# Optimization experiments

Measured on AMD Instinct MI355X. Metric: run time of the kernel, lower is better.

Reference implementation:

```python
import jax, jax.numpy as jnp
import numpy as np

B_, L_, O_, N_, S_, U_, DEL, HID, K = 16, 128, 128, 256, 64, 32, 64, 512, 4
D_OUT = DEL + N_ * U_ + N_ * S_  # 24640


def setup_inputs() -> dict:
    key = jax.random.key(0)
    ks = jax.random.split(key, 12)
    return {
        "x": jax.random.normal(ks[0], (B_, O_ + L_, S_), jnp.float32),
        "u": jax.random.normal(ks[1], (B_, 2 * L_, U_), jnp.float32),
        "A": jax.random.normal(ks[2], (N_, 1), jnp.float32) / 20.0,
        "W0": jax.random.normal(ks[3], (HID, S_), jnp.float32) * 0.05,
        "b0": jnp.zeros((HID,), jnp.float32),
        "W1": jax.random.normal(ks[4], (N_, HID), jnp.float32) * 0.05,
        "b1": jnp.zeros((N_,), jnp.float32),
        "conv_w": jax.random.normal(ks[5], (N_ + U_, 1, K), jnp.float32) * 0.3,
        "conv_b": jnp.zeros((N_ + U_,), jnp.float32),
        "Wg": jax.random.normal(ks[6], (D_OUT, N_ + U_), jnp.float32) * 0.05,
        "bg": jnp.zeros((D_OUT,), jnp.float32),
        "Wdt": jax.random.normal(ks[7], (N_, DEL), jnp.float32) * 0.05,
        "bdt": jnp.zeros((N_,), jnp.float32),
    }


def reference(x, u, A, W0, b0, W1, b1, conv_w, conv_b, Wg, bg, Wdt, bdt):
    def proj_x(v):  # Linear -> relu -> Linear (project_x)
        return jax.nn.relu(v @ W0.T + b0) @ W1.T + b1

    u = u[:, :, :U_]
    z0 = proj_x(x[:, O_ - 1, :])                       # (B, N)

    # ---- generate_matrices ----
    x_all = proj_x(x[:, :O_ - 1, :])                   # (B, O-1, N)
    u_all = u[:, :O_ - 1, :]                           # (B, O-1, U)
    old = jax.nn.silu(jnp.concatenate([x_all, u_all], axis=2))  # (B, O-1, N+U)
    old = jnp.transpose(old, (0, 2, 1))                # (B, N+U, O-1)
    old = jax.lax.conv_general_dilated(
        old, conv_w, window_strides=(1,), padding=[(K - 1, K - 1)],
        dimension_numbers=("NCH", "OIH", "NCH"), feature_group_count=N_ + U_,
    ) + conv_b[None, :, None]
    old = old[:, :, -L_:]                              # last L timesteps
    old = jax.nn.silu(jnp.transpose(old, (0, 2, 1)))   # (B, L, N+U)
    gen = old @ Wg.T + bg                              # (B, L, delta + N*U + N*S)
    delta, Bm, Cm = jnp.split(gen, [DEL, DEL + N_ * U_], axis=-1)
    delta = jax.nn.softplus(delta @ Wdt.T + bdt)       # (B, L, N)
    Bm = Bm.reshape(B_, L_, N_, U_)
    Cm = Cm.reshape(B_, L_, N_, S_)

    # ---- discretion_matrices ----
    a = A[:, 0]
    a = -jnp.where(a > 0, a, jnp.expm1(a))             # -celu(A), alpha=1
    dA = jnp.exp(delta * a)                            # (B, L, N)
    dB = ((dA - 1.0) * (1.0 / a))[..., None] * Bm      # (B, L, N, U)

    # ---- selective_scan ----
    u0 = u[:, O_ - 1:O_ - 1 + L_, :]                   # (B, L, U)
    xt = x[:, O_:O_ + L_, :]                           # (B, L, S) targets

    def step(z, inp):
        dAi, dBi, ui, Ci, xti = inp
        z = z * dAi + jnp.einsum("bnu,bu->bn", dBi, ui)
        y = jnp.einsum("bns,bn->bs", Ci, z)
        return z, (y, jnp.mean((y - xti) ** 2))

    xs = (
        jnp.swapaxes(dA, 0, 1), jnp.swapaxes(dB, 0, 1),
        jnp.swapaxes(u0, 0, 1), jnp.swapaxes(Cm, 0, 1), jnp.swapaxes(xt, 0, 1),
    )
    _, (ys, ls) = jax.lax.scan(step, z0, xs)
    loss = jnp.sum(ls) / L_
    return loss, jax.lax.stop_gradient(ys)             # ys: (L, B, S), detached as in torch
```

## Files before the change

### kernel.cpp

```cpp
#include <hip/hip_runtime.h>
#include <math.h>

#define B_   16
#define L_   128
#define O_   128
#define N_   256
#define S_   64
#define U_   32
#define DEL_ 64
#define HID_ 512
#define CH_  288
#define M_   2048
#define KD_  288
#define CM_BASE (DEL_ + N_*U_)
#define NSLICE 32

typedef __bf16 bf16_t;
typedef bf16_t bf16x8 __attribute__((ext_vector_type(8)));
typedef float  f32x4  __attribute__((ext_vector_type(4)));

#define AS1(p) ((const __attribute__((address_space(1))) void*)(unsigned long long)(const void*)(p))
#define AS3(p) ((__attribute__((address_space(3))) void*)(unsigned int)(unsigned long long)(const void*)(p))

__device__ __forceinline__ float silu_f(float x){ return x / (1.f + expf(-x)); }
__device__ __forceinline__ float softplus_f(float x){
  return fmaxf(x, 0.f) + log1pf(expf(-fabsf(x)));
}

__device__ __forceinline__ void cvt8(const float* src, bf16_t* dst){
  float4 a = ((const float4*)src)[0];
  float4 b = ((const float4*)src)[1];
  bf16x8 o;
  o[0]=(bf16_t)a.x; o[1]=(bf16_t)a.y; o[2]=(bf16_t)a.z; o[3]=(bf16_t)a.w;
  o[4]=(bf16_t)b.x; o[5]=(bf16_t)b.y; o[6]=(bf16_t)b.z; o[7]=(bf16_t)b.w;
  *(bf16x8*)dst = o;
}

#define CVT_BLOCKS 3465
#define W0_BLOCKS  16
#define W1_BLOCKS  64
#define XB_BLOCKS  64
__global__ void k_prep(const float* __restrict__ Wg, bf16_t* __restrict__ Wgbf,
                       const float* __restrict__ W0, bf16_t* __restrict__ W0bf,
                       const float* __restrict__ W1, bf16_t* __restrict__ W1bf,
                       const float* __restrict__ x,  bf16_t* __restrict__ xbf,
                       float* __restrict__ lossa){
  if (blockIdx.x == 0 && threadIdx.x < 2) lossa[threadIdx.x] = 0.f;
  if (blockIdx.x < CVT_BLOCKS) {
    int i = blockIdx.x*256 + threadIdx.x;
    if (i >= 887040) return;
    cvt8(Wg + (size_t)i*8, Wgbf + (size_t)i*8);
  } else if (blockIdx.x < CVT_BLOCKS + W0_BLOCKS) {
    int i = (blockIdx.x - CVT_BLOCKS)*256 + threadIdx.x;
    if (i >= 4096) return;
    cvt8(W0 + (size_t)i*8, W0bf + (size_t)i*8);
  } else if (blockIdx.x < CVT_BLOCKS + W0_BLOCKS + W1_BLOCKS) {
    int i = (blockIdx.x - CVT_BLOCKS - W0_BLOCKS)*256 + threadIdx.x;
    if (i >= 16384) return;
    cvt8(W1 + (size_t)i*8, W1bf + (size_t)i*8);
  } else {
    int i = (blockIdx.x - CVT_BLOCKS - W0_BLOCKS - W1_BLOCKS)*256 + threadIdx.x;
    if (i >= 16384) return;
    int m = i >> 3, c0 = (i & 7)*8;
    int b = m >> 7, t = m & 127;
    cvt8(x + (size_t)(((b<<8)+t)<<6) + c0, xbf + (size_t)m*64 + c0);
  }
}

#define STAGE64K(GBASE, ROW0G, STRIDE, KK, LDSP)                                     \
  { const bf16_t* gp_ = (GBASE) + (size_t)((ROW0G) + wave*16 + lm)*(STRIDE) + (KK) + lq*8; \
    __builtin_amdgcn_global_load_lds(AS1(gp_), AS3((LDSP) + wave*512), 16, 0, 0); }

#define STAGE32(GBASE, ROW0G, KK, LDSP)                                              \
  { _Pragma("unroll")                                                                \
    for (int l_ = 0; l_ < 2; l_++) {                                                 \
      int g_ = wave*2 + l_;                                                          \
      const bf16_t* gp_ = (GBASE) + (size_t)((ROW0G) + g_*16 + lm)*KD_ + (KK) + lq*8;\
      __builtin_amdgcn_global_load_lds(AS1(gp_), AS3((LDSP) + g_*512), 16, 0, 0);    \
    } }

#define STAGE_FR96(GBASE, ROW0G, KK, LDSP)                                           \
  { _Pragma("unroll")                                                                \
    for (int c_ = 0; c_ < 3; c_++) {                                                 \
      _Pragma("unroll")                                                              \
      for (int q_ = 0; q_ < 2; q_++) {                                               \
        int g_ = wave*2 + q_;                                                        \
        const bf16_t* gp_ = (GBASE) + (size_t)((ROW0G) + g_*16 + lm)*KD_ + (KK) + c_*32 + lq*8;\
        __builtin_amdgcn_global_load_lds(AS1(gp_), AS3((LDSP) + c_*4096 + g_*512), 16, 0, 0);\
      } } }

__global__ __launch_bounds__(256) void k_mlp1m(
    const bf16_t* __restrict__ xbf, const bf16_t* __restrict__ W0bf,
    const float* __restrict__ b0, bf16_t* __restrict__ Hbf){
  __shared__ __align__(16) bf16_t As[2][2048];
  __shared__ __align__(16) bf16_t Bs[2][2048];
  int tid = threadIdx.x;
  int wave = tid >> 6, lane = tid & 63;
  int wm = wave & 1, wn = wave >> 1;
  int nt = blockIdx.x, mt = blockIdx.y;
  int m0 = mt*64, n0 = nt*64;
  int lm = lane & 15, lq = lane >> 4;

  f32x4 acc[2][2];
  #pragma unroll
  for (int i=0;i<2;i++)
    #pragma unroll
    for (int j=0;j<2;j++){ acc[i][j][0]=0.f;acc[i][j][1]=0.f;acc[i][j][2]=0.f;acc[i][j][3]=0.f; }

  STAGE64K(xbf,  m0, 64, 0, As[0]);
  STAGE64K(W0bf, n0, 64, 0, Bs[0]);
  __syncthreads();
  #pragma unroll
  for (int t = 0; t < 2; ++t) {
    int cur = t & 1;
    if (t < 1) {
      STAGE64K(xbf,  m0, 64, 32, As[1]);
      STAGE64K(W0bf, n0, 64, 32, Bs[1]);
    }
    bf16x8 af[2], bff[2];
    #pragma unroll
    for (int i=0;i<2;i++) af[i]  = *(const bf16x8*)&As[cur][(wm*2 + i)*512 + lane*8];
    #pragma unroll
    for (int j=0;j<2;j++) bff[j] = *(const bf16x8*)&Bs[cur][(wn*2 + j)*512 + lane*8];
    #pragma unroll
    for (int i=0;i<2;i++)
      #pragma unroll
      for (int j=0;j<2;j++)
        acc[i][j] = __builtin_amdgcn_mfma_f32_16x16x32_bf16(af[i], bff[j], acc[i][j], 0,0,0);
    __syncthreads();
  }
  #pragma unroll
  for (int i=0;i<2;i++)
    #pragma unroll
    for (int j=0;j<2;j++){
      int col = n0 + wn*32 + j*16 + lm;
      float bb = b0[col];
      #pragma unroll
      for (int r=0;r<4;r++){
        int row = m0 + wm*32 + i*16 + lq*4 + r;
        Hbf[(size_t)row*HID_ + col] = (bf16_t)fmaxf(acc[i][j][r] + bb, 0.f);
      }
    }
}

__global__ __launch_bounds__(256) void k_mlp2m(
    const bf16_t* __restrict__ Hbf, const bf16_t* __restrict__ W1bf,
    const float* __restrict__ b1, float* __restrict__ P){
  __shared__ __align__(16) bf16_t As[2][2048];
  __shared__ __align__(16) bf16_t Bs[2][2048];
  int tid = threadIdx.x;
  int wave = tid >> 6, lane = tid & 63;
  int wm = wave & 1, wn = wave >> 1;
  int nt = blockIdx.x, mt = blockIdx.y;
  int m0 = mt*64, n0 = nt*64;
  int lm = lane & 15, lq = lane >> 4;

  f32x4 acc[2][2];
  #pragma unroll
  for (int i=0;i<2;i++)
    #pragma unroll
    for (int j=0;j<2;j++){ acc[i][j][0]=0.f;acc[i][j][1]=0.f;acc[i][j][2]=0.f;acc[i][j][3]=0.f; }

  STAGE64K(Hbf,  m0, HID_, 0, As[0]);
  STAGE64K(W1bf, n0, HID_, 0, Bs[0]);
  __syncthreads();
  for (int t = 0; t < 16; ++t) {
    int cur = t & 1;
    if (t < 15) {
      int kk = (t+1)*32;
      STAGE64K(Hbf,  m0, HID_, kk, As[cur^1]);
      STAGE64K(W1bf, n0, HID_, kk, Bs[cur^1]);
    }
    bf16x8 af[2], bff[2];
    #pragma unroll
    for (int i=0;i<2;i++) af[i]  = *(const bf16x8*)&As[cur][(wm*2 + i)*512 + lane*8];
    #pragma unroll
    for (int j=0;j<2;j++) bff[j] = *(const bf16x8*)&Bs[cur][(wn*2 + j)*512 + lane*8];
    #pragma unroll
    for (int i=0;i<2;i++)
      #pragma unroll
      for (int j=0;j<2;j++)
        acc[i][j] = __builtin_amdgcn_mfma_f32_16x16x32_bf16(af[i], bff[j], acc[i][j], 0,0,0);
    __syncthreads();
  }
  #pragma unroll
  for (int i=0;i<2;i++)
    #pragma unroll
    for (int j=0;j<2;j++){
      int col = n0 + wn*32 + j*16 + lm;
      float bb = b1[col];
      #pragma unroll
      for (int r=0;r<4;r++){
        int row = m0 + wm*32 + i*16 + lq*4 + r;
        P[(size_t)row*N_ + col] = acc[i][j][r] + bb;
      }
    }
}

__global__ __launch_bounds__(256) void k_convdelta(
    const float* __restrict__ P, const float* __restrict__ u,
    const float* __restrict__ cw, const float* __restrict__ cb,
    const float* __restrict__ Wg, const float* __restrict__ bg,
    const float* __restrict__ Wdt, const float* __restrict__ bdt,
    const float* __restrict__ Ap, bf16_t* __restrict__ oldbf,
    float* __restrict__ dA, float* __restrict__ coef){
  __shared__ __align__(16) float olds[4*KD_];
  __shared__ float dr[4][64];
  int tid = threadIdx.x;
  int m0 = blockIdx.x * 4;
  int b = m0 >> 7, l0 = m0 & 127;
  for (int e = tid; e < 4*CH_; e += 256) {
    int r = e / CH_, c = e - r*CH_;
    int l = l0 + r;
    float acc = cb[c];
    #pragma unroll
    for (int k = 0; k < 4; k++) {
      int t = l + k - 1;
      if (t >= 0 && t <= O_-2) {
        float s = (c < N_) ? P[((b<<7)+t)*N_ + c] : u[((b<<8)+t)*U_ + (c-N_)];
        acc += silu_f(s) * cw[c*4 + k];
      }
    }
    float v = silu_f(acc);
    olds[e] = v;
    oldbf[(size_t)(m0+r)*CH_ + c] = (bf16_t)v;
  }
  __syncthreads();
  {
    int d = tid & 63;
    int r = tid >> 6;
    const float* wrow = Wg + (size_t)d*KD_;
    const float* orow = olds + r*KD_;
    float s = 0.f;
    for (int k = 0; k < KD_; k++) s += orow[k] * wrow[k];
    dr[r][d] = s + bg[d];
  }
  __syncthreads();
  int n = tid;
  float wrow[64];
  #pragma unroll
  for (int d = 0; d < 64; d++) wrow[d] = Wdt[n*64 + d];
  float a0 = Ap[n];
  float a = -(a0 > 0.f ? a0 : expm1f(a0));
  float inva = 1.f / a;
  float bd = bdt[n];
  #pragma unroll
  for (int r = 0; r < 4; r++) {
    float s = bd;
    #pragma unroll
    for (int d = 0; d < 64; d++) s += dr[r][d] * wrow[d];
    float dd = softplus_f(s);
    float e  = expf(dd * a);
    size_t m = m0 + r;
    dA[m*N_ + n]   = e;
    coef[m*N_ + n] = (e - 1.f) * inva;
  }
}

__global__ __launch_bounds__(256, 2) void k_bmfma(
    const bf16_t* __restrict__ oldbf, const bf16_t* __restrict__ Wgbf,
    const float* __restrict__ bg, const float* __restrict__ u,
    const float* __restrict__ coef, const float* __restrict__ dAg,
    const float* __restrict__ Pg, float* __restrict__ zall){
  __shared__ union {
    struct { __align__(16) bf16_t A[2][4096]; __align__(16) bf16_t B[2][4096]; } st;
    struct { float wl[128][4]; float dal[128][4]; } sc;
  } sm;
  int tid = threadIdx.x;
  int wave = tid >> 6, lane = tid & 63;
  int wm = wave & 1, wn = wave >> 1;
  int mt = blockIdx.y, nt = blockIdx.x;
  int m0 = mt*128, ncol0 = nt*128;
  int lm = lane & 15, lq = lane >> 4;

  f32x4 acc[4][4];
  #pragma unroll
  for (int i=0;i<4;i++)
    #pragma unroll
    for (int j=0;j<4;j++){ acc[i][j][0]=0.f;acc[i][j][1]=0.f;acc[i][j][2]=0.f;acc[i][j][3]=0.f; }

  STAGE32(oldbf, m0, 0, sm.st.A[0]);
  STAGE32(Wgbf, DEL_ + ncol0, 0, sm.st.B[0]);
  __syncthreads();
  for (int t = 0; t < 9; ++t) {
    int cur = t & 1;
    if (t < 8) {
      int kk = (t+1)*32;
      STAGE32(oldbf, m0, kk, sm.st.A[cur^1]);
      STAGE32(Wgbf, DEL_ + ncol0, kk, sm.st.B[cur^1]);
    }
    bf16x8 af[4], bff[4];
    #pragma unroll
    for (int i=0;i<4;i++) af[i]  = *(const bf16x8*)&sm.st.A[cur][(wm*4 + i)*512 + lane*8];
    #pragma unroll
    for (int j=0;j<4;j++) bff[j] = *(const bf16x8*)&sm.st.B[cur][(wn*4 + j)*512 + lane*8];
    __builtin_amdgcn_s_setprio(1);
    #pragma unroll
    for (int i=0;i<4;i++)
      #pragma unroll
      for (int j=0;j<4;j++)
        acc[i][j] = __builtin_amdgcn_mfma_f32_16x16x32_bf16(af[i], bff[j], acc[i][j], 0,0,0);
    __builtin_amdgcn_s_setprio(0);
    __syncthreads();
  }

  for (int e = tid; e < 512; e += 256)
    sm.sc.dal[e>>2][e&3] = dAg[(size_t)(m0 + (e>>2))*N_ + nt*4 + (e&3)];

  float bgv[4];
  #pragma unroll
  for (int j=0;j<4;j++) bgv[j] = bg[DEL_ + ncol0 + wn*64 + j*16 + lm];
  float p[2][4][4];
  #pragma unroll
  for (int a=0;a<2;a++)
    #pragma unroll
    for (int i=0;i<4;i++)
      #pragma unroll
      for (int r=0;r<4;r++) p[a][i][r]=0.f;
  #pragma unroll
  for (int i=0;i<4;i++){
    #pragma unroll
    for (int r=0;r<4;r++){
      int m = m0 + wm*64 + i*16 + lq*4 + r;
      int b = m >> 7, l = m & 127;
      const float* urow = u + ((size_t)(b<<8) + 127 + l)*U_;
      #pragma unroll
      for (int j=0;j<4;j++){
        float uu = urow[(j&1)*16 + lm];
        p[j>>1][i][r] += (acc[i][j][r] + bgv[j]) * uu;
      }
    }
  }
  #pragma unroll
  for (int mk = 1; mk < 16; mk <<= 1){
    #pragma unroll
    for (int a=0;a<2;a++)
      #pragma unroll
      for (int i=0;i<4;i++)
        #pragma unroll
        for (int r=0;r<4;r++) p[a][i][r] += __shfl_xor(p[a][i][r], mk);
  }
  if (lm == 0){
    #pragma unroll
    for (int nl=0;nl<2;nl++){
      int n = ((ncol0 + wn*64 + nl*32) >> 5);
      int nc = wn*2 + nl;
      #pragma unroll
      for (int i=0;i<4;i++)
        #pragma unroll
        for (int r=0;r<4;r++){
          int l = wm*64 + i*16 + lq*4 + r;
          sm.sc.wl[l][nc] = coef[(size_t)(m0+l)*N_ + n] * p[nl][i][r];
        }
    }
  }
  __syncthreads();

  {
    int nc = wave;
    int n = nt*4 + nc;
    float z0 = Pg[(size_t)(m0 + 127)*N_ + n];
    int l0 = lane*2;
    float a0 = sm.sc.dal[l0][nc],   w0 = sm.sc.wl[l0][nc];
    float a1 = sm.sc.dal[l0+1][nc], w1 = sm.sc.wl[l0+1][nc];
    float A = a0*a1, Bv = w0*a1 + w1;
    #pragma unroll
    for (int d = 1; d < 64; d <<= 1){
      float Ap = __shfl_up(A, d);
      float Bp = __shfl_up(Bv, d);
      if (lane >= d){ Bv = Bp*A + Bv; A = Ap*A; }
    }
    float Ae = __shfl_up(A, 1);
    float Be = __shfl_up(Bv, 1);
    if (lane == 0){ Ae = 1.f; Be = 0.f; }
    float zp = z0*Ae + Be;
    float za = zp*a0 + w0;
    float zb = za*a1 + w1;
    zall[(size_t)(m0 + l0)*N_ + n]     = za;
    zall[(size_t)(m0 + l0 + 1)*N_ + n] = zb;
  }
}

__global__ __launch_bounds__(256, 2) void k_cmfma(
    const bf16_t* __restrict__ oldbf, const bf16_t* __restrict__ Wgbf,
    const float* __restrict__ bg, const float* __restrict__ zall,
    float* __restrict__ ypart){
  __shared__ union {
    struct { __align__(16) bf16_t A[3*4096];
             __align__(16) bf16_t Bb[3*4096];
             float zl[128][8]; } st;
    float ylds[128][64];
  } sm;
  int tid = threadIdx.x;
  int wave = tid >> 6, lane = tid & 63;
  int wm = wave & 1, wn = wave >> 1;
  int mt = blockIdx.y, grp = blockIdx.x;
  int m0 = mt*128;
  int lm = lane & 15, lq = lane >> 4;

  for (int e = tid; e < 1024; e += 256)
    sm.st.zl[e>>3][e&7] = zall[(size_t)(m0 + (e>>3))*N_ + grp*8 + (e&7)];

  f32x4 yacc[4][4];
  #pragma unroll
  for (int i=0;i<4;i++)
    #pragma unroll
    for (int j=0;j<4;j++){ yacc[i][j][0]=0.f;yacc[i][j][1]=0.f;yacc[i][j][2]=0.f;yacc[i][j][3]=0.f; }

  for (int kh = 0; kh < 3; kh++) {
    int kk = kh*96;
    STAGE_FR96(oldbf, m0, kk, sm.st.A);
    for (int it = 0; it < 4; it++) {
      int ncol0 = (grp*4 + it)*128;
      STAGE_FR96(Wgbf, CM_BASE + ncol0, kk, sm.st.Bb);
      __syncthreads();
      f32x4 acc[4][4];
      #pragma unroll
      for (int i=0;i<4;i++)
        #pragma unroll
        for (int j=0;j<4;j++){ acc[i][j][0]=0.f;acc[i][j][1]=0.f;acc[i][j][2]=0.f;acc[i][j][3]=0.f; }
      __builtin_amdgcn_s_setprio(1);
      for (int c = 0; c < 3; c++) {
        bf16x8 af[4], bff[4];
        #pragma unroll
        for (int i=0;i<4;i++) af[i]  = *(const bf16x8*)&sm.st.A[c*4096 + (wm*4 + i)*512 + lane*8];
        #pragma unroll
        for (int j=0;j<4;j++) bff[j] = *(const bf16x8*)&sm.st.Bb[c*4096 + (wn*4 + j)*512 + lane*8];
        #pragma unroll
        for (int i=0;i<4;i++)
          #pragma unroll
          for (int j=0;j<4;j++)
            acc[i][j] = __builtin_amdgcn_mfma_f32_16x16x32_bf16(af[i], bff[j], acc[i][j], 0,0,0);
      }
      __builtin_amdgcn_s_setprio(0);
      int nl = it*2 + wn;
      float bgv[4];
      #pragma unroll
      for (int j=0;j<4;j++)
        bgv[j] = (kh == 2) ? bg[CM_BASE + ncol0 + wn*64 + j*16 + lm] : 0.f;
      #pragma unroll
      for (int i=0;i<4;i++){
        #pragma unroll
        for (int r=0;r<4;r++){
          float zv = sm.st.zl[wm*64 + i*16 + lq*4 + r][nl];
          #pragma unroll
          for (int j=0;j<4;j++)
            yacc[i][j][r] += (acc[i][j][r] + bgv[j]) * zv;
        }
      }
      __syncthreads();
    }
  }

  if (wn == 1){
    #pragma unroll
    for (int i=0;i<4;i++)
      #pragma unroll
      for (int j=0;j<4;j++)
        #pragma unroll
        for (int r=0;r<4;r++){
          int ml = wm*64 + i*16 + lq*4 + r;
          sm.ylds[ml][j*16 + lm] = yacc[i][j][r];
        }
  }
  __syncthreads();
  if (wn == 0){
    float* dst = ypart + (size_t)grp*(M_*S_);
    #pragma unroll
    for (int i=0;i<4;i++)
      #pragma unroll
      for (int j=0;j<4;j++)
        #pragma unroll
        for (int r=0;r<4;r++){
          int ml = wm*64 + i*16 + lq*4 + r;
          int s = j*16 + lm;
          dst[(size_t)(m0+ml)*S_ + s] = yacc[i][j][r] + sm.ylds[ml][s];
        }
  }
}

__global__ void k_finalize(const float* __restrict__ ypart, const float* __restrict__ x,
                           float* __restrict__ out, float* __restrict__ lossacc){
  __shared__ float red[256];
  int tid = threadIdx.x;
  float ls = 0.f;
  #pragma unroll
  for (int q = 0; q < 2; q++) {
    int e = blockIdx.x*512 + q*256 + tid;
    int m = e >> 6, s = e & 63;
    int b = m >> 7, l = m & 127;
    float yv = 0.f;
    #pragma unroll 8
    for (int g = 0; g < NSLICE; g++) yv += ypart[(size_t)g*(M_*S_) + e];
    out[1 + (size_t)((l<<4) + b)*S_ + s] = yv;
    float xv = x[((size_t)(b<<8) + 128 + l)*S_ + s];
    float d = yv - xv;
    ls += d*d;
  }
  red[tid] = ls; __syncthreads();
  for (int st = 128; st > 0; st >>= 1) {
    if (tid < st) red[tid] += red[tid+st];
    __syncthreads();
  }
  if (tid == 0) {
    atomicAdd(&lossacc[0], red[0]);
    __threadfence();
    unsigned old = atomicAdd((unsigned*)&lossacc[1], 1u);
    if (old == 255u) {
      float tot = atomicAdd(&lossacc[0], 0.f);
      out[0] = tot * (1.f / (float)(B_*S_*L_));
    }
  }
}

extern "C" void kernel_launch(void* const* d_in, const int* in_sizes, int n_in,
                              void* d_out, int out_size, void* d_ws, size_t ws_size,
                              hipStream_t stream) {
  const float* x   = (const float*)d_in[0];
  const float* u   = (const float*)d_in[1];
  const float* Ap  = (const float*)d_in[2];
  const float* W0  = (const float*)d_in[3];
  const float* b0  = (const float*)d_in[4];
  const float* W1  = (const float*)d_in[5];
  const float* b1  = (const float*)d_in[6];
  const float* cw  = (const float*)d_in[7];
  const float* cb  = (const float*)d_in[8];
  const float* Wg  = (const float*)d_in[9];
  const float* bg  = (const float*)d_in[10];
  const float* Wdt = (const float*)d_in[11];
  const float* bdt = (const float*)d_in[12];
  float* out = (float*)d_out;

  float* ws    = (float*)d_ws;
  float* zall  = ws;
  float* lossa = zall + 524288;
  bf16_t* oldbf = (bf16_t*)(lossa + 512);
  bf16_t* Wgbf  = (bf16_t*)(lossa + 512 + 294912);
  bf16_t* W0bf  = (bf16_t*)(lossa + 512 + 294912 + 3548160);
  bf16_t* W1bf  = (bf16_t*)(lossa + 512 + 294912 + 3548160 + 16384);
  bf16_t* xbf   = (bf16_t*)(lossa + 512 + 294912 + 3548160 + 16384 + 65536);
  bf16_t* Hbf   = (bf16_t*)(lossa + 512 + 294912 + 3548160 + 16384 + 65536 + 65536);
  float* R     = lossa + 512 + 294912 + 3548160 + 16384 + 65536 + 65536 + 524288;
  float* Pp    = R;
  float* dA    = Pp   + 524288;
  float* coef  = dA   + 524288;
  float* ypart = R;

  k_prep<<<CVT_BLOCKS + W0_BLOCKS + W1_BLOCKS + XB_BLOCKS, 256, 0, stream>>>(
      Wg, Wgbf, W0, W0bf, W1, W1bf, x, xbf, lossa);
  k_mlp1m<<<dim3(HID_/64, M_/64), 256, 0, stream>>>(xbf, W0bf, b0, Hbf);
  k_mlp2m<<<dim3(N_/64, M_/64), 256, 0, stream>>>(Hbf, W1bf, b1, Pp);
  k_convdelta<<<M_/4, 256, 0, stream>>>(Pp, u, cw, cb, Wg, bg, Wdt, bdt, Ap,
                                        oldbf, dA, coef);
  k_bmfma<<<dim3(64, 16), 256, 0, stream>>>(oldbf, Wgbf, bg, u, coef, dA, Pp, zall);
  k_cmfma<<<dim3(32, 16), 256, 0, stream>>>(oldbf, Wgbf, bg, zall, ypart);
  k_finalize<<<256, 256, 0, stream>>>(ypart, x, out, lossa);
}
```

Measured before the change: 203.3 us.

## Merge pipeline stages into two persistent cooperative kernels with grid syncs

Replaces the seven separate kernel launches with two cooperative persistent kernels, k_front (prep + two MLP GEMMs) and k_core (conv/delta, B-scan, C GEMM, finalize). Stages are separated by grid.sync and blocks loop over the original tile indices. The aim is to cut launch overhead and inter-kernel gaps. In exchange, grids are capped by occupancy, so stages with more tiles than resident blocks run serially. Grid barriers and a large shared-memory union could reduce occupancy, and the original kernels remain as a fallback path.

Result: slower. 557.3 us (+174.1%).

```diff
diff --git a/kernel.cpp b/kernel.cpp
--- a/kernel.cpp
+++ b/kernel.cpp
@@ -1,5 +1,8 @@
 #include <hip/hip_runtime.h>
+#include <hip/hip_cooperative_groups.h>
 #include <math.h>
+
+namespace cg = cooperative_groups;
 
 #define B_   16
 #define L_   128
@@ -40,6 +43,467 @@
 #define W0_BLOCKS  16
 #define W1_BLOCKS  64
 #define XB_BLOCKS  64
+#define PREP_TOTAL (CVT_BLOCKS + W0_BLOCKS + W1_BLOCKS + XB_BLOCKS)
+
+#define STAGE64K(GBASE, ROW0G, STRIDE, KK, LDSP)                                     \
+  { const bf16_t* gp_ = (GBASE) + (size_t)((ROW0G) + wave*16 + lm)*(STRIDE) + (KK) + lq*8; \
+    __builtin_amdgcn_global_load_lds(AS1(gp_), AS3((LDSP) + wave*512), 16, 0, 0); }
+
+#define STAGE32(GBASE, ROW0G, KK, LDSP)                                              \
+  { _Pragma("unroll")                                                                \
+    for (int l_ = 0; l_ < 2; l_++) {                                                 \
+      int g_ = wave*2 + l_;                                                          \
+      const bf16_t* gp_ = (GBASE) + (size_t)((ROW0G) + g_*16 + lm)*KD_ + (KK) + lq*8;\
+      __builtin_amdgcn_global_load_lds(AS1(gp_), AS3((LDSP) + g_*512), 16, 0, 0);    \
+    } }
+
+#define STAGE_FR96(GBASE, ROW0G, KK, LDSP)                                           \
+  { _Pragma("unroll")                                                                \
+    for (int c_ = 0; c_ < 3; c_++) {                                                 \
+      _Pragma("unroll")                                                              \
+      for (int q_ = 0; q_ < 2; q_++) {                                               \
+        int g_ = wave*2 + q_;                                                        \
+        const bf16_t* gp_ = (GBASE) + (size_t)((ROW0G) + g_*16 + lm)*KD_ + (KK) + c_*32 + lq*8;\
+        __builtin_amdgcn_global_load_lds(AS1(gp_), AS3((LDSP) + c_*4096 + g_*512), 16, 0, 0);\
+      } } }
+
+__global__ __launch_bounds__(256, 2) void k_front(
+    const float* __restrict__ Wg, bf16_t* __restrict__ Wgbf,
+    const float* __restrict__ W0, bf16_t* __restrict__ W0bf,
+    const float* __restrict__ W1, bf16_t* __restrict__ W1bf,
+    const float* __restrict__ x,  bf16_t* __restrict__ xbf,
+    float* __restrict__ lossa,
+    const float* __restrict__ b0, bf16_t* __restrict__ Hbf,
+    const float* __restrict__ b1, float* __restrict__ P){
+  cg::grid_group grid = cg::this_grid();
+  __shared__ __align__(16) bf16_t As[2][2048];
+  __shared__ __align__(16) bf16_t Bs[2][2048];
+  int tid = threadIdx.x;
+  int wave = tid >> 6, lane = tid & 63;
+  int wm = wave & 1, wn = wave >> 1;
+  int lm = lane & 15, lq = lane >> 4;
+  int nb = gridDim.x;
+
+  if (blockIdx.x == 0 && tid < 2) lossa[tid] = 0.f;
+  for (int blk = blockIdx.x; blk < PREP_TOTAL; blk += nb) {
+    if (blk < CVT_BLOCKS) {
+      int i = blk*256 + tid;
+      if (i < 887040) cvt8(Wg + (size_t)i*8, Wgbf + (size_t)i*8);
+    } else if (blk < CVT_BLOCKS + W0_BLOCKS) {
+      int i = (blk - CVT_BLOCKS)*256 + tid;
+      if (i < 4096) cvt8(W0 + (size_t)i*8, W0bf + (size_t)i*8);
+    } else if (blk < CVT_BLOCKS + W0_BLOCKS + W1_BLOCKS) {
+      int i = (blk - CVT_BLOCKS - W0_BLOCKS)*256 + tid;
+      if (i < 16384) cvt8(W1 + (size_t)i*8, W1bf + (size_t)i*8);
+    } else {
+      int i = (blk - CVT_BLOCKS - W0_BLOCKS - W1_BLOCKS)*256 + tid;
+      if (i < 16384) {
+        int m = i >> 3, c0 = (i & 7)*8;
+        int b = m >> 7, t = m & 127;
+        cvt8(x + (size_t)(((b<<8)+t)<<6) + c0, xbf + (size_t)m*64 + c0);
+      }
+    }
+  }
+  grid.sync();
+
+  for (int blk = blockIdx.x; blk < 256; blk += nb) {
+    int nt = blk & 7, mt = blk >> 3;
+    int m0 = mt*64, n0 = nt*64;
+    __syncthreads();
+    f32x4 acc[2][2];
+    #pragma unroll
+    for (int i=0;i<2;i++)
+      #pragma unroll
+      for (int j=0;j<2;j++){ acc[i][j][0]=0.f;acc[i][j][1]=0.f;acc[i][j][2]=0.f;acc[i][j][3]=0.f; }
+    STAGE64K(xbf,  m0, 64, 0, As[0]);
+    STAGE64K(W0bf, n0, 64, 0, Bs[0]);
+    __syncthreads();
+    #pragma unroll
+    for (int t = 0; t < 2; ++t) {
+      int cur = t & 1;
+      if (t < 1) {
+        STAGE64K(xbf,  m0, 64, 32, As[1]);
+        STAGE64K(W0bf, n0, 64, 32, Bs[1]);
+      }
+      bf16x8 af[2], bff[2];
+      #pragma unroll
+      for (int i=0;i<2;i++) af[i]  = *(const bf16x8*)&As[cur][(wm*2 + i)*512 + lane*8];
+      #pragma unroll
+      for (int j=0;j<2;j++) bff[j] = *(const bf16x8*)&Bs[cur][(wn*2 + j)*512 + lane*8];
+      #pragma unroll
+      for (int i=0;i<2;i++)
+        #pragma unroll
+        for (int j=0;j<2;j++)
+          acc[i][j] = __builtin_amdgcn_mfma_f32_16x16x32_bf16(af[i], bff[j], acc[i][j], 0,0,0);
+      __syncthreads();
+    }
+    #pragma unroll
+    for (int i=0;i<2;i++)
+      #pragma unroll
+      for (int j=0;j<2;j++){
+        int col = n0 + wn*32 + j*16 + lm;
+        float bb = b0[col];
+        #pragma unroll
+        for (int r=0;r<4;r++){
+          int row = m0 + wm*32 + i*16 + lq*4 + r;
+          Hbf[(size_t)row*HID_ + col] = (bf16_t)fmaxf(acc[i][j][r] + bb, 0.f);
+        }
+      }
+  }
+  grid.sync();
+
+  for (int blk = blockIdx.x; blk < 128; blk += nb) {
+    int nt = blk & 3, mt = blk >> 2;
+    int m0 = mt*64, n0 = nt*64;
+    __syncthreads();
+    f32x4 acc[2][2];
+    #pragma unroll
+    for (int i=0;i<2;i++)
+      #pragma unroll
+      for (int j=0;j<2;j++){ acc[i][j][0]=0.f;acc[i][j][1]=0.f;acc[i][j][2]=0.f;acc[i][j][3]=0.f; }
+    STAGE64K(Hbf,  m0, HID_, 0, As[0]);
+    STAGE64K(W1bf, n0, HID_, 0, Bs[0]);
+    __syncthreads();
+    for (int t = 0; t < 16; ++t) {
+      int cur = t & 1;
+      if (t < 15) {
+        int kk = (t+1)*32;
+        STAGE64K(Hbf,  m0, HID_, kk, As[cur^1]);
+        STAGE64K(W1bf, n0, HID_, kk, Bs[cur^1]);
+      }
+      bf16x8 af[2], bff[2];
+      #pragma unroll
+      for (int i=0;i<2;i++) af[i]  = *(const bf16x8*)&As[cur][(wm*2 + i)*512 + lane*8];
+      #pragma unroll
+      for (int j=0;j<2;j++) bff[j] = *(const bf16x8*)&Bs[cur][(wn*2 + j)*512 + lane*8];
+      #pragma unroll
+      for (int i=0;i<2;i++)
+        #pragma unroll
+        for (int j=0;j<2;j++)
+          acc[i][j] = __builtin_amdgcn_mfma_f32_16x16x32_bf16(af[i], bff[j], acc[i][j], 0,0,0);
+      __syncthreads();
+    }
+    #pragma unroll
+    for (int i=0;i<2;i++)
+      #pragma unroll
+      for (int j=0;j<2;j++){
+        int col = n0 + wn*32 + j*16 + lm;
+        float bb = b1[col];
+        #pragma unroll
+        for (int r=0;r<4;r++){
+          int row = m0 + wm*32 + i*16 + lq*4 + r;
+          P[(size_t)row*N_ + col] = acc[i][j][r] + bb;
+        }
+      }
+  }
+}
+
+__global__ __launch_bounds__(256, 2) void k_core(
+    const float* __restrict__ P, const float* __restrict__ uu,
+    const float* __restrict__ cw, const float* __restrict__ cb,
+    const float* __restrict__ Wg, const float* __restrict__ bg,
+    const float* __restrict__ Wdt, const float* __restrict__ bdt,
+    const float* __restrict__ Ap, bf16_t* __restrict__ oldbf,
+    float* __restrict__ dA, float* __restrict__ coef,
+    const bf16_t* __restrict__ Wgbf, float* __restrict__ zall,
+    float* __restrict__ ypart, const float* __restrict__ x,
+    float* __restrict__ out, float* __restrict__ lossa){
+  cg::grid_group grid = cg::this_grid();
+  __shared__ union {
+    struct { __align__(16) float olds[4*KD_]; float dr[4][64]; } cv;
+    struct { __align__(16) bf16_t A[2][4096]; __align__(16) bf16_t B[2][4096];
+             float wl[128][4]; float dal[128][4]; } bm;
+    union {
+      struct { __align__(16) bf16_t A[3*4096]; __align__(16) bf16_t Bb[3*4096];
+               float zl[128][8]; } st;
+      float ylds[128][64];
+    } cm;
+    float red[256];
+  } sm;
+  int tid = threadIdx.x;
+  int wave = tid >> 6, lane = tid & 63;
+  int wm = wave & 1, wn = wave >> 1;
+  int lm = lane & 15, lq = lane >> 4;
+  int nb = gridDim.x;
+
+  for (int blk = blockIdx.x; blk < 512; blk += nb) {
+    int m0 = blk * 4;
+    int b = m0 >> 7, l0 = m0 & 127;
+    __syncthreads();
+    for (int e = tid; e < 4*CH_; e += 256) {
+      int r = e / CH_, c = e - r*CH_;
+      int l = l0 + r;
+      float acc = cb[c];
+      #pragma unroll
+      for (int k = 0; k < 4; k++) {
+        int t = l + k - 1;
+        if (t >= 0 && t <= O_-2) {
+          float s = (c < N_) ? P[((b<<7)+t)*N_ + c] : uu[((b<<8)+t)*U_ + (c-N_)];
+          acc += silu_f(s) * cw[c*4 + k];
+        }
+      }
+      float v = silu_f(acc);
+      sm.cv.olds[e] = v;
+      oldbf[(size_t)(m0+r)*CH_ + c] = (bf16_t)v;
+    }
+    __syncthreads();
+    {
+      int d = tid & 63;
+      int r = tid >> 6;
+      const float* wrow = Wg + (size_t)d*KD_;
+      const float* orow = sm.cv.olds + r*KD_;
+      float s = 0.f;
+      for (int k = 0; k < KD_; k++) s += orow[k] * wrow[k];
+      sm.cv.dr[r][d] = s + bg[d];
+    }
+    __syncthreads();
+    int n = tid;
+    float wrow[64];
+    #pragma unroll
+    for (int d = 0; d < 64; d++) wrow[d] = Wdt[n*64 + d];
+    float a0 = Ap[n];
+    float a = -(a0 > 0.f ? a0 : expm1f(a0));
+    float inva = 1.f / a;
+    float bd = bdt[n];
+    #pragma unroll
+    for (int r = 0; r < 4; r++) {
+      float s = bd;
+      #pragma unroll
+      for (int d = 0; d < 64; d++) s += sm.cv.dr[r][d] * wrow[d];
+      float dd = softplus_f(s);
+      float e  = expf(dd * a);
+      size_t m = m0 + r;
+      dA[m*N_ + n]   = e;
+      coef[m*N_ + n] = (e - 1.f) * inva;
+    }
+  }
+  grid.sync();
+
+  for (int blk = blockIdx.x; blk < 1024; blk += nb) {
+    int nt = blk & 63, mt = blk >> 6;
+    int m0 = mt*128, ncol0 = nt*128;
+    __syncthreads();
+    f32x4 acc[4][4];
+    #pragma unroll
+    for (int i=0;i<4;i++)
+      #pragma unroll
+      for (int j=0;j<4;j++){ acc[i][j][0]=0.f;acc[i][j][1]=0.f;acc[i][j][2]=0.f;acc[i][j][3]=0.f; }
+    STAGE32(oldbf, m0, 0, sm.bm.A[0]);
+    STAGE32(Wgbf, DEL_ + ncol0, 0, sm.bm.B[0]);
+    __syncthreads();
+    for (int t = 0; t < 9; ++t) {
+      int cur = t & 1;
+      if (t < 8) {
+        int kk = (t+1)*32;
+        STAGE32(oldbf, m0, kk, sm.bm.A[cur^1]);
+        STAGE32(Wgbf, DEL_ + ncol0, kk, sm.bm.B[cur^1]);
+      }
+      bf16x8 af[4], bff[4];
+      #pragma unroll
+      for (int i=0;i<4;i++) af[i]  = *(const bf16x8*)&sm.bm.A[cur][(wm*4 + i)*512 + lane*8];
+      #pragma unroll
+      for (int j=0;j<4;j++) bff[j] = *(const bf16x8*)&sm.bm.B[cur][(wn*4 + j)*512 + lane*8];
+      __builtin_amdgcn_s_setprio(1);
+      #pragma unroll
+      for (int i=0;i<4;i++)
+        #pragma unroll
+        for (int j=0;j<4;j++)
+          acc[i][j] = __builtin_amdgcn_mfma_f32_16x16x32_bf16(af[i], bff[j], acc[i][j], 0,0,0);
+      __builtin_amdgcn_s_setprio(0);
+      __syncthreads();
+    }
+    for (int e = tid; e < 512; e += 256)
+      sm.bm.dal[e>>2][e&3] = dA[(size_t)(m0 + (e>>2))*N_ + nt*4 + (e&3)];
+    float bgv[4];
+    #pragma unroll
+    for (int j=0;j<4;j++) bgv[j] = bg[DEL_ + ncol0 + wn*64 + j*16 + lm];
+    float p[2][4][4];
+    #pragma unroll
+    for (int a=0;a<2;a++)
+      #pragma unroll
+      for (int i=0;i<4;i++)
+        #pragma unroll
+        for (int r=0;r<4;r++) p[a][i][r]=0.f;
+    #pragma unroll
+    for (int i=0;i<4;i++){
+      #pragma unroll
+      for (int r=0;r<4;r++){
+        int m = m0 + wm*64 + i*16 + lq*4 + r;
+        int b = m >> 7, l = m & 127;
+        const float* urow = uu + ((size_t)(b<<8) + 127 + l)*U_;
+        #pragma unroll
+        for (int j=0;j<4;j++){
+          float uv = urow[(j&1)*16 + lm];
+          p[j>>1][i][r] += (acc[i][j][r] + bgv[j]) * uv;
+        }
+      }
+    }
+    #pragma unroll
+    for (int mk = 1; mk < 16; mk <<= 1){
+      #pragma unroll
+      for (int a=0;a<2;a++)
+        #pragma unroll
+        for (int i=0;i<4;i++)
+          #pragma unroll
+          for (int r=0;r<4;r++) p[a][i][r] += __shfl_xor(p[a][i][r], mk);
+    }
+    if (lm == 0){
+      #pragma unroll
+      for (int nl=0;nl<2;nl++){
+        int n = ((ncol0 + wn*64 + nl*32) >> 5);
+        int nc = wn*2 + nl;
+        #pragma unroll
+        for (int i=0;i<4;i++)
+          #pragma unroll
+          for (int r=0;r<4;r++){
+            int l = wm*64 + i*16 + lq*4 + r;
+            sm.bm.wl[l][nc] = coef[(size_t)(m0+l)*N_ + n] * p[nl][i][r];
+          }
+      }
+    }
+    __syncthreads();
+    {
+      int nc = wave;
+      int n = nt*4 + nc;
+      float z0 = P[(size_t)(m0 + 127)*N_ + n];
+      int l0 = lane*2;
+      float a0 = sm.bm.dal[l0][nc],   w0 = sm.bm.wl[l0][nc];
+      float a1 = sm.bm.dal[l0+1][nc], w1 = sm.bm.wl[l0+1][nc];
+      float A = a0*a1, Bv = w0*a1 + w1;
+      #pragma unroll
+      for (int d = 1; d < 64; d <<= 1){
+        float Apx = __shfl_up(A, d);
+        float Bpx = __shfl_up(Bv, d);
+        if (lane >= d){ Bv = Bpx*A + Bv; A = Apx*A; }
+      }
+      float Ae = __shfl_up(A, 1);
+      float Be = __shfl_up(Bv, 1);
+      if (lane == 0){ Ae = 1.f; Be = 0.f; }
+      float zp = z0*Ae + Be;
+      float za = zp*a0 + w0;
+      float zb = za*a1 + w1;
+      zall[(size_t)(m0 + l0)*N_ + n]     = za;
+      zall[(size_t)(m0 + l0 + 1)*N_ + n] = zb;
+    }
+  }
+  grid.sync();
+
+  for (int blk = blockIdx.x; blk < 512; blk += nb) {
+    int grp = blk & 31, mt = blk >> 5;
+    int m0 = mt*128;
+    __syncthreads();
+    for (int e = tid; e < 1024; e += 256)
+      sm.cm.st.zl[e>>3][e&7] = zall[(size_t)(m0 + (e>>3))*N_ + grp*8 + (e&7)];
+    f32x4 yacc[4][4];
+    #pragma unroll
+    for (int i=0;i<4;i++)
+      #pragma unroll
+      for (int j=0;j<4;j++){ yacc[i][j][0]=0.f;yacc[i][j][1]=0.f;yacc[i][j][2]=0.f;yacc[i][j][3]=0.f; }
+    for (int kh = 0; kh < 3; kh++) {
+      int kk = kh*96;
+      STAGE_FR96(oldbf, m0, kk, sm.cm.st.A);
+      for (int it = 0; it < 4; it++) {
+        int ncol0 = (grp*4 + it)*128;
+        STAGE_FR96(Wgbf, CM_BASE + ncol0, kk, sm.cm.st.Bb);
+        __syncthreads();
+        f32x4 acc[4][4];
+        #pragma unroll
+        for (int i=0;i<4;i++)
+          #pragma unroll
+          for (int j=0;j<4;j++){ acc[i][j][0]=0.f;acc[i][j][1]=0.f;acc[i][j][2]=0.f;acc[i][j][3]=0.f; }
+        __builtin_amdgcn_s_setprio(1);
+        for (int c = 0; c < 3; c++) {
+          bf16x8 af[4], bff[4];
+          #pragma unroll
+          for (int i=0;i<4;i++) af[i]  = *(const bf16x8*)&sm.cm.st.A[c*4096 + (wm*4 + i)*512 + lane*8];
+          #pragma unroll
+          for (int j=0;j<4;j++) bff[j] = *(const bf16x8*)&sm.cm.st.Bb[c*4096 + (wn*4 + j)*512 + lane*8];
+          #pragma unroll
+          for (int i=0;i<4;i++)
+            #pragma unroll
+            for (int j=0;j<4;j++)
+              acc[i][j] = __builtin_amdgcn_mfma_f32_16x16x32_bf16(af[i], bff[j], acc[i][j], 0,0,0);
+        }
+        __builtin_amdgcn_s_setprio(0);
+        int nl = it*2 + wn;
+        float bgv[4];
+        #pragma unroll
+        for (int j=0;j<4;j++)
+          bgv[j] = (kh == 2) ? bg[CM_BASE + ncol0 + wn*64 + j*16 + lm] : 0.f;
+        #pragma unroll
+        for (int i=0;i<4;i++){
+          #pragma unroll
+          for (int r=0;r<4;r++){
+            float zv = sm.cm.st.zl[wm*64 + i*16 + lq*4 + r][nl];
+            #pragma unroll
+            for (int j=0;j<4;j++)
+              yacc[i][j][r] += (acc[i][j][r] + bgv[j]) * zv;
+          }
+        }
+        __syncthreads();
+      }
+    }
+    if (wn == 1){
+      #pragma unroll
+      for (int i=0;i<4;i++)
+        #pragma unroll
+        for (int j=0;j<4;j++)
+          #pragma unroll
+          for (int r=0;r<4;r++){
+            int ml = wm*64 + i*16 + lq*4 + r;
+            sm.cm.ylds[ml][j*16 + lm] = yacc[i][j][r];
+          }
+    }
+    __syncthreads();
+    if (wn == 0){
+      float* dst = ypart + (size_t)grp*(M_*S_);
+      #pragma unroll
+      for (int i=0;i<4;i++)
+        #pragma unroll
+        for (int j=0;j<4;j++)
+          #pragma unroll
+          for (int r=0;r<4;r++){
+            int ml = wm*64 + i*16 + lq*4 + r;
+            int s = j*16 + lm;
+            dst[(size_t)(m0+ml)*S_ + s] = yacc[i][j][r] + sm.cm.ylds[ml][s];
+          }
+    }
+  }
+  grid.sync();
+
+  for (int blk = blockIdx.x; blk < 256; blk += nb) {
+    __syncthreads();
+    float ls = 0.f;
+    #pragma unroll
+    for (int q = 0; q < 2; q++) {
+      int e = blk*512 + q*256 + tid;
+      int m = e >> 6, s = e & 63;
+      int b = m >> 7, l = m & 127;
+      float yv = 0.f;
+      #pragma unroll 8
+      for (int g = 0; g < NSLICE; g++) yv += ypart[(size_t)g*(M_*S_) + e];
+      out[1 + (size_t)((l<<4) + b)*S_ + s] = yv;
+      float xv = x[((size_t)(b<<8) + 128 + l)*S_ + s];
+      float d = yv - xv;
+      ls += d*d;
+    }
+    sm.red[tid] = ls; __syncthreads();
+    for (int st = 128; st > 0; st >>= 1) {
+      if (tid < st) sm.red[tid] += sm.red[tid+st];
+      __syncthreads();
+    }
+    if (tid == 0) {
+      atomicAdd(&lossa[0], sm.red[0]);
+      __threadfence();
+      unsigned old = atomicAdd((unsigned*)&lossa[1], 1u);
+      if (old == 255u) {
+        float tot = atomicAdd(&lossa[0], 0.f);
+        out[0] = tot * (1.f / (float)(B_*S_*L_));
+      }
+    }
+  }
+}
+
 __global__ void k_prep(const float* __restrict__ Wg, bf16_t* __restrict__ Wgbf,
                        const float* __restrict__ W0, bf16_t* __restrict__ W0bf,
                        const float* __restrict__ W1, bf16_t* __restrict__ W1bf,
@@ -67,28 +531,6 @@
   }
 }
 
-#define STAGE64K(GBASE, ROW0G, STRIDE, KK, LDSP)                                     \
-  { const bf16_t* gp_ = (GBASE) + (size_t)((ROW0G) + wave*16 + lm)*(STRIDE) + (KK) + lq*8; \
-    __builtin_amdgcn_global_load_lds(AS1(gp_), AS3((LDSP) + wave*512), 16, 0, 0); }
-
-#define STAGE32(GBASE, ROW0G, KK, LDSP)                                              \
-  { _Pragma("unroll")                                                                \
-    for (int l_ = 0; l_ < 2; l_++) {                                                 \
-      int g_ = wave*2 + l_;                                                          \
-      const bf16_t* gp_ = (GBASE) + (size_t)((ROW0G) + g_*16 + lm)*KD_ + (KK) + lq*8;\
-      __builtin_amdgcn_global_load_lds(AS1(gp_), AS3((LDSP) + g_*512), 16, 0, 0);    \
-    } }
-
-#define STAGE_FR96(GBASE, ROW0G, KK, LDSP)                                           \
-  { _Pragma("unroll")                                                                \
-    for (int c_ = 0; c_ < 3; c_++) {                                                 \
-      _Pragma("unroll")                                                              \
-      for (int q_ = 0; q_ < 2; q_++) {                                               \
-        int g_ = wave*2 + q_;                                                        \
-        const bf16_t* gp_ = (GBASE) + (size_t)((ROW0G) + g_*16 + lm)*KD_ + (KK) + c_*32 + lq*8;\
-        __builtin_amdgcn_global_load_lds(AS1(gp_), AS3((LDSP) + c_*4096 + g_*512), 16, 0, 0);\
-      } } }
-
 __global__ __launch_bounds__(256) void k_mlp1m(
     const bf16_t* __restrict__ xbf, const bf16_t* __restrict__ W0bf,
     const float* __restrict__ b0, bf16_t* __restrict__ Hbf){
@@ -100,13 +542,11 @@
   int nt = blockIdx.x, mt = blockIdx.y;
   int m0 = mt*64, n0 = nt*64;
   int lm = lane & 15, lq = lane >> 4;
-
   f32x4 acc[2][2];
   #pragma unroll
   for (int i=0;i<2;i++)
     #pragma unroll
     for (int j=0;j<2;j++){ acc[i][j][0]=0.f;acc[i][j][1]=0.f;acc[i][j][2]=0.f;acc[i][j][3]=0.f; }
-
   STAGE64K(xbf,  m0, 64, 0, As[0]);
   STAGE64K(W0bf, n0, 64, 0, Bs[0]);
   __syncthreads();
@@ -154,13 +594,11 @@
   int nt = blockIdx.x, mt = blockIdx.y;
   int m0 = mt*64, n0 = nt*64;
   int lm = lane & 15, lq = lane >> 4;
-
   f32x4 acc[2][2];
   #pragma unroll
   for (int i=0;i<2;i++)
     #pragma unroll
     for (int j=0;j<2;j++){ acc[i][j][0]=0.f;acc[i][j][1]=0.f;acc[i][j][2]=0.f;acc[i][j][3]=0.f; }
-
   STAGE64K(Hbf,  m0, HID_, 0, As[0]);
   STAGE64K(W1bf, n0, HID_, 0, Bs[0]);
   __syncthreads();
@@ -272,13 +710,11 @@
   int mt = blockIdx.y, nt = blockIdx.x;
   int m0 = mt*128, ncol0 = nt*128;
   int lm = lane & 15, lq = lane >> 4;
-
   f32x4 acc[4][4];
   #pragma unroll
   for (int i=0;i<4;i++)
     #pragma unroll
     for (int j=0;j<4;j++){ acc[i][j][0]=0.f;acc[i][j][1]=0.f;acc[i][j][2]=0.f;acc[i][j][3]=0.f; }
-
   STAGE32(oldbf, m0, 0, sm.st.A[0]);
   STAGE32(Wgbf, DEL_ + ncol0, 0, sm.st.B[0]);
   __syncthreads();
@@ -303,10 +739,8 @@
     __builtin_amdgcn_s_setprio(0);
     __syncthreads();
   }
-
   for (int e = tid; e < 512; e += 256)
     sm.sc.dal[e>>2][e&3] = dAg[(size_t)(m0 + (e>>2))*N_ + nt*4 + (e&3)];
-
   float bgv[4];
   #pragma unroll
   for (int j=0;j<4;j++) bgv[j] = bg[DEL_ + ncol0 + wn*64 + j*16 + lm];
@@ -326,8 +760,8 @@
       const float* urow = u + ((size_t)(b<<8) + 127 + l)*U_;
       #pragma unroll
       for (int j=0;j<4;j++){
-        float uu = urow[(j&1)*16 + lm];
-        p[j>>1][i][r] += (acc[i][j][r] + bgv[j]) * uu;
+        float uv = urow[(j&1)*16 + lm];
+        p[j>>1][i][r] += (acc[i][j][r] + bgv[j]) * uv;
       }
     }
   }
@@ -355,7 +789,6 @@
     }
   }
   __syncthreads();
-
   {
     int nc = wave;
     int n = nt*4 + nc;
@@ -366,9 +799,9 @@
     float A = a0*a1, Bv = w0*a1 + w1;
     #pragma unroll
     for (int d = 1; d < 64; d <<= 1){
-      float Ap = __shfl_up(A, d);
-      float Bp = __shfl_up(Bv, d);
-      if (lane >= d){ Bv = Bp*A + Bv; A = Ap*A; }
+      float Apx = __shfl_up(A, d);
+      float Bpx = __shfl_up(Bv, d);
+      if (lane >= d){ Bv = Bpx*A + Bv; A = Apx*A; }
     }
     float Ae = __shfl_up(A, 1);
     float Be = __shfl_up(Bv, 1);
@@ -397,16 +830,13 @@
   int mt = blockIdx.y, grp = blockIdx.x;
   int m0 = mt*128;
   int lm = lane & 15, lq = lane >> 4;
-
   for (int e = tid; e < 1024; e += 256)
     sm.st.zl[e>>3][e&7] = zall[(size_t)(m0 + (e>>3))*N_ + grp*8 + (e&7)];
-
   f32x4 yacc[4][4];
   #pragma unroll
   for (int i=0;i<4;i++)
     #pragma unroll
     for (int j=0;j<4;j++){ yacc[i][j][0]=0.f;yacc[i][j][1]=0.f;yacc[i][j][2]=0.f;yacc[i][j][3]=0.f; }
-
   for (int kh = 0; kh < 3; kh++) {
     int kk = kh*96;
     STAGE_FR96(oldbf, m0, kk, sm.st.A);
@@ -451,7 +881,6 @@
       __syncthreads();
     }
   }
-
   if (wn == 1){
     #pragma unroll
     for (int i=0;i<4;i++)
@@ -546,13 +975,43 @@
   float* coef  = dA   + 524288;
   float* ypart = R;
 
-  k_prep<<<CVT_BLOCKS + W0_BLOCKS + W1_BLOCKS + XB_BLOCKS, 256, 0, stream>>>(
-      Wg, Wgbf, W0, W0bf, W1, W1bf, x, xbf, lossa);
-  k_mlp1m<<<dim3(HID_/64, M_/64), 256, 0, stream>>>(xbf, W0bf, b0, Hbf);
-  k_mlp2m<<<dim3(N_/64, M_/64), 256, 0, stream>>>(Hbf, W1bf, b1, Pp);
-  k_convdelta<<<M_/4, 256, 0, stream>>>(Pp, u, cw, cb, Wg, bg, Wdt, bdt, Ap,
-                                        oldbf, dA, coef);
-  k_bmfma<<<dim3(64, 16), 256, 0, stream>>>(oldbf, Wgbf, bg, u, coef, dA, Pp, zall);
-  k_cmfma<<<dim3(32, 16), 256, 0, stream>>>(oldbf, Wgbf, bg, zall, ypart);
-  k_finalize<<<256, 256, 0, stream>>>(ypart, x, out, lossa);
-}
+  static int occ_front = -2, occ_core = -2;
+  if (occ_front == -2) {
+    if (hipOccupancyMaxActiveBlocksPerMultiprocessor(&occ_front,
+          reinterpret_cast<const void*>(&k_front), 256, 0) != hipSuccess) occ_front = 0;
+    if (hipOccupancyMaxActiveBlocksPerMultiprocessor(&occ_core,
+          reinterpret_cast<const void*>(&k_core), 256, 0) != hipSuccess) occ_core = 0;
+  }
+  int grid_f = occ_front > 0 ? min(2048, occ_front*256) : 0;
+  int grid_c = occ_core  > 0 ? min(512,  occ_core*256)  : 0;
+
+  bool front_ok = false, core_ok = false;
+  if (grid_f > 0) {
+    void* fa[] = { (void*)&Wg, (void*)&Wgbf, (void*)&W0, (void*)&W0bf,
+                   (void*)&W1, (void*)&W1bf, (void*)&x, (void*)&xbf,
+                   (void*)&lossa, (void*)&b0, (void*)&Hbf, (void*)&b1, (void*)&Pp };
+    front_ok = (hipLaunchCooperativeKernel(reinterpret_cast<const void*>(&k_front),
+                 dim3(grid_f), dim3(256), fa, 0, stream) == hipSuccess);
+  }
+  if (!front_ok) {
+    k_prep<<<PREP_TOTAL, 256, 0, stream>>>(Wg, Wgbf, W0, W0bf, W1, W1bf, x, xbf, lossa);
+    k_mlp1m<<<dim3(HID_/64, M_/64), 256, 0, stream>>>(xbf, W0bf, b0, Hbf);
+    k_mlp2m<<<dim3(N_/64, M_/64), 256, 0, stream>>>(Hbf, W1bf, b1, Pp);
+  }
+  if (grid_c > 0) {
+    void* ca[] = { (void*)&Pp, (void*)&u, (void*)&cw, (void*)&cb,
+                   (void*)&Wg, (void*)&bg, (void*)&Wdt, (void*)&bdt,
+                   (void*)&Ap, (void*)&oldbf, (void*)&dA, (void*)&coef,
+                   (void*)&Wgbf, (void*)&zall, (void*)&ypart, (void*)&x,
+                   (void*)&out, (void*)&lossa };
+    core_ok = (hipLaunchCooperativeKernel(reinterpret_cast<const void*>(&k_core),
+                dim3(grid_c), dim3(256), ca, 0, stream) == hipSuccess);
+  }
+  if (!core_ok) {
+    k_convdelta<<<M_/4, 256, 0, stream>>>(Pp, u, cw, cb, Wg, bg, Wdt, bdt, Ap,
+                                          oldbf, dA, coef);
+    k_bmfma<<<dim3(64, 16), 256, 0, stream>>>(oldbf, Wgbf, bg, u, coef, dA, Pp, zall);
+    k_cmfma<<<dim3(32, 16), 256, 0, stream>>>(oldbf, Wgbf, bg, zall, ypart);
+    k_finalize<<<256, 256, 0, stream>>>(ypart, x, out, lossa);
+  }
+}
```
